# Kernel optimization log

Measured on AMD Instinct MI355X. Metric: run time of the kernel, lower is better.

## Reference

```python
import jax, jax.numpy as jnp
import numpy as np

B, T1, T2, C, H, NIN = 4, 4096, 2048, 512, 8, 3
D = C // H  # head_dim = 64


def setup_inputs() -> dict:
    key = jax.random.key(0)
    ks = jax.random.split(key, 10)
    s = 0.02  # weight init scale
    return {
        "x": jax.random.normal(ks[0], (B, T1, C), jnp.float32),
        "y0": jax.random.normal(ks[1], (B, T2, C), jnp.float32),
        "y1": jax.random.normal(ks[2], (B, T2, C), jnp.float32),
        "y2": jax.random.normal(ks[3], (B, T2, C), jnp.float32),
        "Wq": jax.random.normal(ks[4], (C, C), jnp.float32) * s,
        "bq": jnp.zeros((C,), jnp.float32),
        "Wk": jax.random.normal(ks[5], (NIN, C, C), jnp.float32) * s,
        "bk": jnp.zeros((NIN, C), jnp.float32),
        "Wv": jax.random.normal(ks[6], (NIN, C, C), jnp.float32) * s,
        "bv": jnp.zeros((NIN, C), jnp.float32),
        "Wo": jax.random.normal(ks[7], (C, C), jnp.float32) * s,
        "bo": jnp.zeros((C,), jnp.float32),
    }


def _heads(t, n_head):
    b, n, c = t.shape
    return t.reshape(b, n, n_head, c // n_head).transpose(0, 2, 1, 3)  # [B,H,N,D]


def reference(x, y0, y1, y2, Wq, bq, Wk, bk, Wv, bv, Wo, bo):
    b, t1, c = x.shape
    q = jax.nn.softmax(_heads(x @ Wq.T + bq, H), axis=-1)  # [B,H,T1,D]
    out = q  # note: original initializes accumulator with q itself
    for i, y in enumerate((y0, y1, y2)):
        k = jax.nn.softmax(_heads(y @ Wk[i].T + bk[i], H), axis=-1)  # [B,H,T2,D]
        v = _heads(y @ Wv[i].T + bv[i], H)                            # [B,H,T2,D]
        k_sum = k.sum(axis=-2, keepdims=True)                         # [B,H,1,D]
        D_inv = 1.0 / ((q * k_sum).sum(axis=-1, keepdims=True) + 1e-8)  # [B,H,T1,1]
        context = jnp.einsum('bhnd,bhnv->bhdv', k, v)                 # [B,H,D,D]
        out = out + jnp.einsum('bhqd,bhdv->bhqv', q, context) * D_inv
    out = out.transpose(0, 2, 1, 3).reshape(b, t1, c)
    return out @ Wo.T + bo
```

## Files before the change

kernel.cpp:

```cpp
#include <hip/hip_runtime.h>
#include <stdint.h>

#define B_ 4
#define T1_ 4096
#define T2_ 2048
#define C_ 512
#define H_ 8
#define D_ 64
#define M1_ (B_*T1_)
#define M2_ (B_*T2_)

using f32x4 = __attribute__((ext_vector_type(4))) float;
using bf16x8 = __attribute__((ext_vector_type(8))) __bf16;
using us8 = __attribute__((ext_vector_type(8))) unsigned short;
using us4 = __attribute__((ext_vector_type(4))) unsigned short;

__device__ __forceinline__ unsigned short f2bf(float f){
  unsigned int u = __builtin_bit_cast(unsigned int, f);
  unsigned int r = (u + 0x7fffu + ((u >> 16) & 1u)) >> 16;
  return (unsigned short)r;
}
__device__ __forceinline__ float bf2f(unsigned short u){
  return __builtin_bit_cast(float, ((unsigned int)u) << 16);
}
__device__ __forceinline__ f32x4 mfma16(us8 a, us8 b, f32x4 c){
  return __builtin_amdgcn_mfma_f32_16x16x32_bf16(
      __builtin_bit_cast(bf16x8, a), __builtin_bit_cast(bf16x8, b), c, 0, 0, 0);
}
__device__ __forceinline__ us8 cvt8(f32x4 a, f32x4 b){
  us8 v;
  #pragma unroll
  for (int j = 0; j < 4; ++j){
    v[j]   = __builtin_bit_cast(unsigned short, (__bf16)a[j]);
    v[4+j] = __builtin_bit_cast(unsigned short, (__bf16)b[j]);
  }
  return v;
}

typedef const __attribute__((address_space(1))) unsigned int gu32;
typedef __attribute__((address_space(3))) unsigned int lu32;
__device__ __forceinline__ void gl_lds16(const void* g, void* l){
  __builtin_amdgcn_global_load_lds((gu32*)g, (lu32*)l, 16, 0, 0);
}

#define WAIT_VM(N) asm volatile("s_waitcnt vmcnt(" #N ")" ::: "memory")
#define WAIT_LGKM() asm volatile("s_waitcnt lgkmcnt(0)" ::: "memory")
#define RAW_BAR()  { __builtin_amdgcn_s_barrier(); __builtin_amdgcn_sched_barrier(0); }

__device__ __forceinline__ int swz(int row, int blk){ return blk ^ ((row >> 1) & 3); }

__global__ __launch_bounds__(256) void cvt_bf16_4(const float* __restrict__ p0, const float* __restrict__ p1,
                                                  const float* __restrict__ p2, const float* __restrict__ p3,
                                                  unsigned short* o0, unsigned short* o1,
                                                  unsigned short* o2, unsigned short* o3,
                                                  int n0, int n1, int n2, int n3){
  const float* in; unsigned short* out; int n4;
  switch (blockIdx.y){
    case 0: in = p0; out = o0; n4 = n0; break;
    case 1: in = p1; out = o1; n4 = n1; break;
    case 2: in = p2; out = o2; n4 = n2; break;
    default: in = p3; out = o3; n4 = n3; break;
  }
  int i = blockIdx.x * 256 + threadIdx.x;
  if (i >= n4) return;
  f32x4 v = ((const f32x4*)in)[i];
  us4 o;
  #pragma unroll
  for (int j = 0; j < 4; ++j) o[j] = f2bf(v[j]);
  ((us4*)out)[i] = o;
}

__device__ __forceinline__ void tile_write(unsigned short* tile, const f32x4 (&vals)[4][4],
                                           int wr, int wc, int lr, int lk){
  #pragma unroll
  for (int mt = 0; mt < 4; ++mt)
    #pragma unroll
    for (int nt = 0; nt < 4; ++nt)
      #pragma unroll
      for (int r = 0; r < 4; ++r){
        int row = wr*64 + mt*16 + lk*4 + r;
        int cb  = (wc*128 + nt*32 + lr*2) ^ ((row & 7) << 4);
        *(unsigned short*)((char*)tile + row*256 + cb) = f2bf(vals[mt][nt][r]);
      }
}
__device__ __forceinline__ void tile_write_T(unsigned short* tile, const f32x4 (&vals)[4][4],
                                             int wr, int wc, int lr, int lk){
  #pragma unroll
  for (int mt = 0; mt < 4; ++mt)
    #pragma unroll
    for (int nt = 0; nt < 4; ++nt)
      #pragma unroll
      for (int r = 0; r < 4; ++r){
        int n  = wr*64 + mt*16 + lk*4 + r;
        int ch = wc*64 + nt*16 + lr;
        int cb = (n*2) ^ ((ch & 7) << 4);
        *(unsigned short*)((char*)tile + ch*256 + cb) = f2bf(vals[mt][nt][r]);
      }
}
__device__ __forceinline__ void tile_flush(const unsigned short* tile, unsigned short* g,
                                           size_t row0, int col0, int ldg, int t){
  #pragma unroll
  for (int p = 0; p < 8; ++p){
    int row = p*16 + (t >> 4);
    int cb  = ((t & 15) * 16) ^ ((row & 7) << 4);
    us8 v = *(const us8*)((const char*)tile + row*256 + cb);
    *(us8*)(g + (row0 + row) * (size_t)ldg + col0 + (t & 15) * 8) = v;
  }
}

__global__ __launch_bounds__(256, 3) void proj(const float* __restrict__ xf,
                                               const float* __restrict__ y0f,
                                               const float* __restrict__ y1f,
                                               const float* __restrict__ y2f,
                                               const unsigned short* __restrict__ wqb,
                                               const unsigned short* __restrict__ wkb,
                                               const unsigned short* __restrict__ wvb,
                                               const float* __restrict__ bq,
                                               const float* __restrict__ bk,
                                               const float* __restrict__ bv,
                                               unsigned short* __restrict__ qb,
                                               unsigned short* __restrict__ kbT,
                                               unsigned short* __restrict__ vbT,
                                               float* __restrict__ ksum){
  __shared__ unsigned short smem[24576];
  const int hw = blockIdx.x;
  const int work = (hw & 7) * 256 + (hw >> 3);
  int seg, ii, m0, n0;
  const float* Af;
  const unsigned short* W;
  const float* bias;
  if (work < 512){
    seg = 0; ii = 0;
    m0 = (work >> 2) << 7; n0 = (work & 3) << 7;
    Af = xf; W = wqb; bias = bq;
  } else {
    int r = work - 512;
    int g = r >> 3, s = r & 7;
    ii = g >> 6; m0 = (g & 63) << 7;
    seg = (s < 4) ? 1 : 2;
    n0 = (s & 3) << 7;
    Af = (ii == 0) ? y0f : (ii == 1 ? y1f : y2f);
    W = (seg == 1 ? wkb : wvb) + (size_t)ii*C_*C_;
    bias = (seg == 1 ? bk : bv) + (size_t)ii*C_;
  }
  const int t = threadIdx.x;
  const int w = t >> 6, l = t & 63;
  const int wr = w >> 1, wc = w & 1;
  const int lr = l & 15, lk = l >> 4;
  const int row0 = t >> 2,          b0 = t & 3;
  const int row1 = (t + 256) >> 2,  b1 = t & 3;
  f32x4 acc[4][4] = {};
  f32x4 ar0[4], ar1[4];

#define LOADA(AR, TT) { \
    const float* ap0 = Af + (size_t)(m0+row0)*C_ + (TT)*32 + b0*8; \
    const float* ap1 = Af + (size_t)(m0+row1)*C_ + (TT)*32 + b1*8; \
    AR[0] = *(const f32x4*)ap0; AR[1] = *(const f32x4*)(ap0 + 4); \
    AR[2] = *(const f32x4*)ap1; AR[3] = *(const f32x4*)(ap1 + 4); }
#define DSWA(AR, BUF) { \
    *(us8*)&smem[(BUF)*4096 + row0*32 + swz(row0,b0)*8] = cvt8(AR[0], AR[1]); \
    *(us8*)&smem[(BUF)*4096 + row1*32 + swz(row1,b1)*8] = cvt8(AR[2], AR[3]); }
#define GLW(BUF, TT) { \
    int c=t, row=c>>2; \
    gl_lds16(W + (size_t)(n0+row)*C_ + (TT)*32 + swz(row,c&3)*8, &smem[12288+(BUF)*4096 + c*8]); \
    c=t+256; row=c>>2; \
    gl_lds16(W + (size_t)(n0+row)*C_ + (TT)*32 + swz(row,c&3)*8, &smem[12288+(BUF)*4096 + c*8]); }
#define PCOMP(S, WB) { \
    const unsigned short* sA = &smem[(S)*4096]; \
    const unsigned short* sW = &smem[12288 + (WB)*4096]; \
    us8 af[4], bfr[4]; \
    _Pragma("unroll") \
    for (int mt = 0; mt < 4; ++mt){ int R = wr*64 + mt*16 + lr; af[mt] = *(const us8*)&sA[R*32 + swz(R, lk)*8]; } \
    _Pragma("unroll") \
    for (int nt = 0; nt < 4; ++nt){ int R = wc*64 + nt*16 + lr; bfr[nt] = *(const us8*)&sW[R*32 + swz(R, lk)*8]; } \
    __builtin_amdgcn_s_setprio(1); \
    _Pragma("unroll") \
    for (int mt = 0; mt < 4; ++mt) \
      _Pragma("unroll") \
      for (int nt = 0; nt < 4; ++nt) \
        acc[mt][nt] = mfma16(af[mt], bfr[nt], acc[mt][nt]); \
    __builtin_amdgcn_s_setprio(0); }
#define PSTEP(T, ARW, ARL) { \
    WAIT_VM(2); \
    DSWA(ARW, ((T)+1)%3); \
    LOADA(ARL, (T)+2); \
    GLW(((T)+2)%3, (T)+2); \
    PCOMP((T)%3, (T)%3); \
    WAIT_LGKM(); \
    WAIT_VM(6); \
    RAW_BAR(); }

  LOADA(ar0, 0); GLW(0, 0);
  LOADA(ar1, 1); GLW(1, 1);
  WAIT_VM(8);
  DSWA(ar0, 0);
  WAIT_LGKM();
  WAIT_VM(6);
  RAW_BAR();
  PSTEP(0,  ar1, ar0) PSTEP(1,  ar0, ar1) PSTEP(2,  ar1, ar0) PSTEP(3,  ar0, ar1)
  PSTEP(4,  ar1, ar0) PSTEP(5,  ar0, ar1) PSTEP(6,  ar1, ar0) PSTEP(7,  ar0, ar1)
  PSTEP(8,  ar1, ar0) PSTEP(9,  ar0, ar1) PSTEP(10, ar1, ar0) PSTEP(11, ar0, ar1)
  PSTEP(12, ar1, ar0) PSTEP(13, ar0, ar1)
  {
    WAIT_VM(2);
    DSWA(ar1, 0);
    PCOMP(2, 2);
    WAIT_LGKM();
    WAIT_VM(0);
    RAW_BAR();
  }
  PCOMP(0, 0);
#undef LOADA
#undef DSWA
#undef GLW
#undef PCOMP
#undef PSTEP

  {
    float bc[4];
    #pragma unroll
    for (int nt = 0; nt < 4; ++nt) bc[nt] = bias[n0 + wc*64 + nt*16 + lr];
    #pragma unroll
    for (int mt = 0; mt < 4; ++mt)
      #pragma unroll
      for (int nt = 0; nt < 4; ++nt)
        #pragma unroll
        for (int r = 0; r < 4; ++r) acc[mt][nt][r] += bc[nt];
  }
  if (seg <= 1){
    #pragma unroll
    for (int mt = 0; mt < 4; ++mt)
      #pragma unroll
      for (int r = 0; r < 4; ++r){
        float m = fmaxf(fmaxf(acc[mt][0][r], acc[mt][1][r]), fmaxf(acc[mt][2][r], acc[mt][3][r]));
        #pragma unroll
        for (int s = 1; s < 16; s <<= 1) m = fmaxf(m, __shfl_xor(m, s, 64));
        float sum = 0.f;
        #pragma unroll
        for (int nt = 0; nt < 4; ++nt){
          float e = __expf(acc[mt][nt][r] - m);
          acc[mt][nt][r] = e; sum += e;
        }
        #pragma unroll
        for (int s = 1; s < 16; s <<= 1) sum += __shfl_xor(sum, s, 64);
        float inv = 1.0f / sum;
        #pragma unroll
        for (int nt = 0; nt < 4; ++nt) acc[mt][nt][r] *= inv;
      }
  }
  if (seg == 1){
    const int b = m0 >> 11;
    #pragma unroll
    for (int nt = 0; nt < 4; ++nt){
      float cs = 0.f;
      #pragma unroll
      for (int mt = 0; mt < 4; ++mt)
        #pragma unroll
        for (int r = 0; r < 4; ++r) cs += acc[mt][nt][r];
      cs += __shfl_xor(cs, 16, 64);
      cs += __shfl_xor(cs, 32, 64);
      if (lk == 0)
        atomicAdd(&ksum[((size_t)ii*B_ + b)*C_ + n0 + wc*64 + nt*16 + lr], cs);
    }
  }
  __syncthreads();
  if (seg == 0){
    tile_write(smem, acc, wr, wc, lr, lk);
    __syncthreads();
    tile_flush(smem, qb, m0, n0, C_, t);
  } else {
    tile_write_T(smem, acc, wr, wc, lr, lk);
    __syncthreads();
    const int b = m0 >> 11;
    const int n_base = m0 & 2047;
    unsigned short* gT = (seg == 1 ? kbT : vbT);
    tile_flush(smem, gT, ((size_t)ii*B_ + b)*C_ + n0, n_base, T2_, t);
  }
}

__global__ __launch_bounds__(256) void ctx_mfma(const unsigned short* __restrict__ kbT,
                                                const unsigned short* __restrict__ vbT,
                                                float* __restrict__ part){
  const int bh = blockIdx.x, kc = blockIdx.y, i = blockIdx.z;
  const int b = bh >> 3, h = bh & 7;
  const size_t rowbase = ((size_t)i*B_ + b)*C_ + h*64;
  const unsigned short* kT = kbT + rowbase*T2_;
  const unsigned short* vT = vbT + rowbase*T2_;
  const int t = threadIdx.x;
  const int w = t >> 6, l = t & 63;
  const int qr = w >> 1, qc = w & 1;
  const int lr = l & 15, lk = l >> 4;
  const int n00 = kc * 256;
  f32x4 acc[2][2] = {};
  #pragma unroll
  for (int it = 0; it < 8; ++it){
    const int k0 = n00 + it*32 + lk*8;
    us8 a0 = *(const us8*)(kT + (size_t)(qr*32 +      lr)*T2_ + k0);
    us8 a1 = *(const us8*)(kT + (size_t)(qr*32 + 16 + lr)*T2_ + k0);
    us8 b0 = *(const us8*)(vT + (size_t)(qc*32 +      lr)*T2_ + k0);
    us8 b1 = *(const us8*)(vT + (size_t)(qc*32 + 16 + lr)*T2_ + k0);
    acc[0][0] = mfma16(a0, b0, acc[0][0]);
    acc[0][1] = mfma16(a0, b1, acc[0][1]);
    acc[1][0] = mfma16(a1, b0, acc[1][0]);
    acc[1][1] = mfma16(a1, b1, acc[1][1]);
  }
  float* dst = part + (((size_t)i*8 + kc)*32 + bh)*4096;
  #pragma unroll
  for (int fa = 0; fa < 2; ++fa)
    #pragma unroll
    for (int fb = 0; fb < 2; ++fb){
      int d0 = qr*32 + fa*16 + lk*4;
      int e  = qc*32 + fb*16 + lr;
      *(f32x4*)(dst + e*64 + d0) = acc[fa][fb];
    }
}

__global__ __launch_bounds__(256) void ctx_reduce(const float* __restrict__ part,
                                                  unsigned short* __restrict__ ctxTb){
  const int bh = blockIdx.x, i = blockIdx.y, t = threadIdx.x;
  for (int idx = t; idx < 4096; idx += 256){
    float s = 0.f;
    #pragma unroll
    for (int kc = 0; kc < 8; ++kc)
      s += part[(((size_t)i*8 + kc)*32 + bh)*4096 + idx];
    ctxTb[((size_t)i*32 + bh)*4096 + idx] = f2bf(s);
  }
}

__global__ __launch_bounds__(256) void combine(const unsigned short* __restrict__ qb,
                                               const unsigned short* __restrict__ ctxTb,
                                               const float* __restrict__ ksum,
                                               unsigned short* __restrict__ omid){
  __shared__ unsigned short tile[128*128];
  const int hw = blockIdx.x;
  const int work = (hw & 7) * 64 + (hw >> 3);
  const int m0 = (work & 127) << 7, n0 = (work >> 7) << 7;
  const int t = threadIdx.x;
  const int w = t >> 6, l = t & 63;
  const int wr = w >> 1, wc = w & 1;
  const int lr = l & 15, lk = l >> 4;
  const int b = m0 >> 12;
  const int bh = b*8 + (n0 >> 6) + wc;
  #pragma unroll
  for (int p = 0; p < 8; ++p){
    int idx = p*256 + t;
    int row = idx >> 4, ch = idx & 15;
    gl_lds16(qb + (size_t)(m0+row)*C_ + n0 + (ch ^ (row & 7))*8, &tile[idx*8]);
  }
  WAIT_VM(0);
  __syncthreads();
  us8 afr[4][2];
  #pragma unroll
  for (int mt = 0; mt < 4; ++mt)
    #pragma unroll
    for (int kk = 0; kk < 2; ++kk){
      int row = wr*64 + mt*16 + lr;
      int ch = wc*8 + kk*4 + lk;
      afr[mt][kk] = *(const us8*)((const char*)tile + row*256 + ((ch ^ (row & 7)) << 4));
    }
  f32x4 acc[4][4];
  #pragma unroll
  for (int mt = 0; mt < 4; ++mt)
    #pragma unroll
    for (int nt = 0; nt < 4; ++nt)
      #pragma unroll
      for (int r = 0; r < 4; ++r){
        int row = wr*64 + mt*16 + lk*4 + r;
        int cbyte = wc*128 + nt*32 + lr*2;
        int ch = cbyte >> 4;
        unsigned short v = *(const unsigned short*)((const char*)tile + row*256 +
                            ((ch ^ (row & 7)) << 4) + (cbyte & 15));
        acc[mt][nt][r] = bf2f(v);
      }
  us8 bden[2];
  #pragma unroll
  for (int kk = 0; kk < 2; ++kk){
    us8 tmp = {};
    if (lr < 3){
      const float* kp = ksum + ((size_t)lr*B_ + b)*C_ + n0 + wc*64 + kk*32 + lk*8;
      f32x4 c0 = *(const f32x4*)kp;
      f32x4 c1 = *(const f32x4*)(kp + 4);
      #pragma unroll
      for (int j = 0; j < 4; ++j){ tmp[j] = f2bf(c0[j]); tmp[4+j] = f2bf(c1[j]); }
    }
    bden[kk] = tmp;
  }
  f32x4 den[4] = {};
  #pragma unroll
  for (int mt = 0; mt < 4; ++mt)
    #pragma unroll
    for (int kk = 0; kk < 2; ++kk)
      den[mt] = mfma16(afr[mt][kk], bden[kk], den[mt]);
  #pragma unroll 1
  for (int i = 0; i < 3; ++i){
    f32x4 dinv[4];
    #pragma unroll
    for (int mt = 0; mt < 4; ++mt)
      #pragma unroll
      for (int r = 0; r < 4; ++r)
        dinv[mt][r] = 1.0f / (__shfl(den[mt][r], (l & 48) | i, 64) + 1e-8f);
    #pragma unroll
    for (int nt = 0; nt < 4; ++nt){
      us8 bfr[2];
      #pragma unroll
      for (int kk = 0; kk < 2; ++kk)
        bfr[kk] = *(const us8*)(ctxTb + ((size_t)(i*32 + bh))*4096 + (nt*16 + lr)*64 + kk*32 + lk*8);
      f32x4 p[4] = {};
      #pragma unroll
      for (int mt = 0; mt < 4; ++mt)
        #pragma unroll
        for (int kk = 0; kk < 2; ++kk)
          p[mt] = mfma16(afr[mt][kk], bfr[kk], p[mt]);
      #pragma unroll
      for (int mt = 0; mt < 4; ++mt)
        #pragma unroll
        for (int r = 0; r < 4; ++r)
          acc[mt][nt][r] += p[mt][r] * dinv[mt][r];
    }
  }
  __syncthreads();
  tile_write(tile, acc, wr, wc, lr, lk);
  __syncthreads();
  tile_flush(tile, omid, m0, n0, C_, t);
}

__global__ __launch_bounds__(256, 3) void gemm_bt(const unsigned short* __restrict__ A,
                                                  const unsigned short* __restrict__ Bw,
                                                  const float* __restrict__ bias,
                                                  float* __restrict__ out){
  __shared__ unsigned short smem[3*2*4096];
  const int hw = blockIdx.x;
  const int work = (hw & 7) * 64 + (hw >> 3);
  const int m0 = ((work >> 2) & 127) << 7, n0 = (work & 3) << 7;
  const int t = threadIdx.x;
  const int w = t >> 6, l = t & 63;
  const int wr = w >> 1, wc = w & 1;
  const int lr = l & 15, lk = l >> 4;
  f32x4 acc[4][4] = {};

#define GSTAGE(BB, TT) { \
    int c = t, row = c >> 2; \
    gl_lds16(A  + (size_t)(m0+row)*C_ + (TT)*32 + swz(row, c & 3)*8, &smem[(BB)*8192 + c*8]); \
    gl_lds16(Bw + (size_t)(n0+row)*C_ + (TT)*32 + swz(row, c & 3)*8, &smem[(BB)*8192 + 4096 + c*8]); \
    c = t + 256; row = c >> 2; \
    gl_lds16(A  + (size_t)(m0+row)*C_ + (TT)*32 + swz(row, c & 3)*8, &smem[(BB)*8192 + c*8]); \
    gl_lds16(Bw + (size_t)(n0+row)*C_ + (TT)*32 + swz(row, c & 3)*8, &smem[(BB)*8192 + 4096 + c*8]); }
#define GCOMP(BB) { \
    const unsigned short* sA = &smem[(BB)*8192]; \
    const unsigned short* sB = &smem[(BB)*8192 + 4096]; \
    us8 af[4], bfr[4]; \
    _Pragma("unroll") \
    for (int mt = 0; mt < 4; ++mt){ int R = wr*64 + mt*16 + lr; af[mt] = *(const us8*)&sA[R*32 + swz(R, lk)*8]; } \
    _Pragma("unroll") \
    for (int nt = 0; nt < 4; ++nt){ int R = wc*64 + nt*16 + lr; bfr[nt] = *(const us8*)&sB[R*32 + swz(R, lk)*8]; } \
    __builtin_amdgcn_s_setprio(1); \
    _Pragma("unroll") \
    for (int mt = 0; mt < 4; ++mt) \
      _Pragma("unroll") \
      for (int nt = 0; nt < 4; ++nt) \
        acc[mt][nt] = mfma16(af[mt], bfr[nt], acc[mt][nt]); \
    __builtin_amdgcn_s_setprio(0); }
#define GSTEP(T, N) { \
    if ((T) + 2 < 16) GSTAGE(((T)+2)%3, (T)+2); \
    WAIT_VM(N); \
    RAW_BAR(); \
    GCOMP((T)%3); }

  GSTAGE(0, 0); GSTAGE(1, 1);
  GSTEP(0, 8)  GSTEP(1, 8)  GSTEP(2, 8)  GSTEP(3, 8)
  GSTEP(4, 8)  GSTEP(5, 8)  GSTEP(6, 8)  GSTEP(7, 8)
  GSTEP(8, 8)  GSTEP(9, 8)  GSTEP(10, 8) GSTEP(11, 8)
  GSTEP(12, 8) GSTEP(13, 8) GSTEP(14, 4) GSTEP(15, 0)
#undef GSTAGE
#undef GCOMP
#undef GSTEP

  #pragma unroll
  for (int mt = 0; mt < 4; ++mt)
    #pragma unroll
    for (int nt = 0; nt < 4; ++nt)
      #pragma unroll
      for (int r = 0; r < 4; ++r){
        int row = m0 + wr*64 + mt*16 + lk*4 + r;
        int col = n0 + wc*64 + nt*16 + lr;
        out[(size_t)row*C_ + col] = acc[mt][nt][r] + bias[col];
      }
}

extern "C" void kernel_launch(void* const* d_in, const int* in_sizes, int n_in,
                              void* d_out, int out_size, void* d_ws, size_t ws_size,
                              hipStream_t stream){
  const float* x  = (const float*)d_in[0];
  const float* y0 = (const float*)d_in[1];
  const float* y1 = (const float*)d_in[2];
  const float* y2 = (const float*)d_in[3];
  const float* Wq = (const float*)d_in[4];
  const float* bq = (const float*)d_in[5];
  const float* Wk = (const float*)d_in[6];
  const float* bk = (const float*)d_in[7];
  const float* Wv = (const float*)d_in[8];
  const float* bv = (const float*)d_in[9];
  const float* Wo = (const float*)d_in[10];
  const float* bo = (const float*)d_in[11];

  char* ws = (char*)d_ws;
  size_t off = 0;
  auto alloc = [&](size_t bytes)->char*{
    char* p = ws + off; off += (bytes + 1023) & ~((size_t)1023); return p;
  };
  unsigned short* wqb   = (unsigned short*)alloc((size_t)C_*C_*2);
  unsigned short* wkb   = (unsigned short*)alloc((size_t)3*C_*C_*2);
  unsigned short* wvb   = (unsigned short*)alloc((size_t)3*C_*C_*2);
  unsigned short* wob   = (unsigned short*)alloc((size_t)C_*C_*2);
  unsigned short* qb    = (unsigned short*)alloc((size_t)M1_*C_*2);
  unsigned short* kbT   = (unsigned short*)alloc((size_t)3*B_*C_*T2_*2);
  unsigned short* vbT   = (unsigned short*)alloc((size_t)3*B_*C_*T2_*2);
  float*          ksum  = (float*)alloc((size_t)3*B_*C_*4);
  float*          part  = (float*)alloc((size_t)3*8*32*4096*4);
  unsigned short* ctxTb = (unsigned short*)alloc((size_t)3*32*4096*2);
  unsigned short* omid  = (unsigned short*)alloc((size_t)M1_*C_*2);

  (void)hipMemsetAsync(ksum, 0, (size_t)3*B_*C_*4, stream);

  cvt_bf16_4<<<dim3(3*C_*C_/4/256, 4), 256, 0, stream>>>(
      Wq, Wk, Wv, Wo, wqb, wkb, wvb, wob,
      C_*C_/4, 3*C_*C_/4, 3*C_*C_/4, C_*C_/4);

  proj<<<2048, 256, 0, stream>>>(x, y0, y1, y2, wqb, wkb, wvb, bq, bk, bv, qb, kbT, vbT, ksum);
  ctx_mfma<<<dim3(32, 8, 3), 256, 0, stream>>>(kbT, vbT, part);
  ctx_reduce<<<dim3(32, 3), 256, 0, stream>>>(part, ctxTb);
  combine<<<512, 256, 0, stream>>>(qb, ctxTb, ksum, omid);
  gemm_bt<<<512, 256, 0, stream>>>(omid, wob, bo, (float*)d_out);
}
```

Before: 123.3 us.

## Stream fp32 A tiles directly to LDS and convert to bf16 at fragment load

Result: slower. 140.5 us (+14.0%).

```diff
diff --git a/kernel.cpp b/kernel.cpp
--- a/kernel.cpp
+++ b/kernel.cpp
@@ -44,7 +44,6 @@
 }
 
 #define WAIT_VM(N) asm volatile("s_waitcnt vmcnt(" #N ")" ::: "memory")
-#define WAIT_LGKM() asm volatile("s_waitcnt lgkmcnt(0)" ::: "memory")
 #define RAW_BAR()  { __builtin_amdgcn_s_barrier(); __builtin_amdgcn_sched_barrier(0); }
 
 __device__ __forceinline__ int swz(int row, int blk){ return blk ^ ((row >> 1) & 3); }
@@ -108,21 +107,21 @@
   }
 }
 
-__global__ __launch_bounds__(256, 3) void proj(const float* __restrict__ xf,
-                                               const float* __restrict__ y0f,
-                                               const float* __restrict__ y1f,
-                                               const float* __restrict__ y2f,
-                                               const unsigned short* __restrict__ wqb,
-                                               const unsigned short* __restrict__ wkb,
-                                               const unsigned short* __restrict__ wvb,
-                                               const float* __restrict__ bq,
-                                               const float* __restrict__ bk,
-                                               const float* __restrict__ bv,
-                                               unsigned short* __restrict__ qb,
-                                               unsigned short* __restrict__ kbT,
-                                               unsigned short* __restrict__ vbT,
-                                               float* __restrict__ ksum){
-  __shared__ unsigned short smem[24576];
+__global__ __launch_bounds__(256) void proj(const float* __restrict__ xf,
+                                            const float* __restrict__ y0f,
+                                            const float* __restrict__ y1f,
+                                            const float* __restrict__ y2f,
+                                            const unsigned short* __restrict__ wqb,
+                                            const unsigned short* __restrict__ wkb,
+                                            const unsigned short* __restrict__ wvb,
+                                            const float* __restrict__ bq,
+                                            const float* __restrict__ bk,
+                                            const float* __restrict__ bv,
+                                            unsigned short* __restrict__ qb,
+                                            unsigned short* __restrict__ kbT,
+                                            unsigned short* __restrict__ vbT,
+                                            float* __restrict__ ksum){
+  __shared__ unsigned short smem[36864];
   const int hw = blockIdx.x;
   const int work = (hw & 7) * 256 + (hw >> 3);
   int seg, ii, m0, n0;
@@ -147,30 +146,30 @@
   const int w = t >> 6, l = t & 63;
   const int wr = w >> 1, wc = w & 1;
   const int lr = l & 15, lk = l >> 4;
-  const int row0 = t >> 2,          b0 = t & 3;
-  const int row1 = (t + 256) >> 2,  b1 = t & 3;
   f32x4 acc[4][4] = {};
-  f32x4 ar0[4], ar1[4];
-
-#define LOADA(AR, TT) { \
-    const float* ap0 = Af + (size_t)(m0+row0)*C_ + (TT)*32 + b0*8; \
-    const float* ap1 = Af + (size_t)(m0+row1)*C_ + (TT)*32 + b1*8; \
-    AR[0] = *(const f32x4*)ap0; AR[1] = *(const f32x4*)(ap0 + 4); \
-    AR[2] = *(const f32x4*)ap1; AR[3] = *(const f32x4*)(ap1 + 4); }
-#define DSWA(AR, BUF) { \
-    *(us8*)&smem[(BUF)*4096 + row0*32 + swz(row0,b0)*8] = cvt8(AR[0], AR[1]); \
-    *(us8*)&smem[(BUF)*4096 + row1*32 + swz(row1,b1)*8] = cvt8(AR[2], AR[3]); }
-#define GLW(BUF, TT) { \
-    int c=t, row=c>>2; \
-    gl_lds16(W + (size_t)(n0+row)*C_ + (TT)*32 + swz(row,c&3)*8, &smem[12288+(BUF)*4096 + c*8]); \
-    c=t+256; row=c>>2; \
-    gl_lds16(W + (size_t)(n0+row)*C_ + (TT)*32 + swz(row,c&3)*8, &smem[12288+(BUF)*4096 + c*8]); }
-#define PCOMP(S, WB) { \
-    const unsigned short* sA = &smem[(S)*4096]; \
-    const unsigned short* sW = &smem[12288 + (WB)*4096]; \
+
+#define STAGE(BB, TT) { \
+    _Pragma("unroll") \
+    for (int j = 0; j < 4; ++j){ \
+      int c = t + j*256, row = c >> 3, ch = c & 7; \
+      gl_lds16(Af + (size_t)(m0+row)*C_ + (TT)*32 + ((ch ^ (row & 7)) << 2), \
+               &smem[(BB)*8192 + c*8]); \
+    } \
+    { int c = t, row = c >> 2; \
+      gl_lds16(W + (size_t)(n0+row)*C_ + (TT)*32 + swz(row, c & 3)*8, &smem[24576 + (BB)*4096 + c*8]); \
+      c = t + 256; row = c >> 2; \
+      gl_lds16(W + (size_t)(n0+row)*C_ + (TT)*32 + swz(row, c & 3)*8, &smem[24576 + (BB)*4096 + c*8]); } }
+#define PCOMP(BB) { \
+    const float* sAf = (const float*)&smem[(BB)*8192]; \
+    const unsigned short* sW = &smem[24576 + (BB)*4096]; \
     us8 af[4], bfr[4]; \
     _Pragma("unroll") \
-    for (int mt = 0; mt < 4; ++mt){ int R = wr*64 + mt*16 + lr; af[mt] = *(const us8*)&sA[R*32 + swz(R, lk)*8]; } \
+    for (int mt = 0; mt < 4; ++mt){ \
+      int R = wr*64 + mt*16 + lr, x = R & 7; \
+      f32x4 a0 = *(const f32x4*)(sAf + R*32 + (((2*lk)     ^ x) << 2)); \
+      f32x4 a1 = *(const f32x4*)(sAf + R*32 + (((2*lk + 1) ^ x) << 2)); \
+      af[mt] = cvt8(a0, a1); \
+    } \
     _Pragma("unroll") \
     for (int nt = 0; nt < 4; ++nt){ int R = wc*64 + nt*16 + lr; bfr[nt] = *(const us8*)&sW[R*32 + swz(R, lk)*8]; } \
     __builtin_amdgcn_s_setprio(1); \
@@ -180,41 +179,23 @@
       for (int nt = 0; nt < 4; ++nt) \
         acc[mt][nt] = mfma16(af[mt], bfr[nt], acc[mt][nt]); \
     __builtin_amdgcn_s_setprio(0); }
-#define PSTEP(T, ARW, ARL) { \
-    WAIT_VM(2); \
-    DSWA(ARW, ((T)+1)%3); \
-    LOADA(ARL, (T)+2); \
-    GLW(((T)+2)%3, (T)+2); \
-    PCOMP((T)%3, (T)%3); \
-    WAIT_LGKM(); \
-    WAIT_VM(6); \
-    RAW_BAR(); }
-
-  LOADA(ar0, 0); GLW(0, 0);
-  LOADA(ar1, 1); GLW(1, 1);
-  WAIT_VM(8);
-  DSWA(ar0, 0);
-  WAIT_LGKM();
-  WAIT_VM(6);
+
+  STAGE(0, 0);
+  int cur = 0;
+  #pragma unroll 1
+  for (int tt = 0; tt < 15; ++tt){
+    int nxt = (cur == 2) ? 0 : cur + 1;
+    STAGE(nxt, tt + 1);
+    WAIT_VM(6);
+    RAW_BAR();
+    PCOMP(cur);
+    cur = nxt;
+  }
+  WAIT_VM(0);
   RAW_BAR();
-  PSTEP(0,  ar1, ar0) PSTEP(1,  ar0, ar1) PSTEP(2,  ar1, ar0) PSTEP(3,  ar0, ar1)
-  PSTEP(4,  ar1, ar0) PSTEP(5,  ar0, ar1) PSTEP(6,  ar1, ar0) PSTEP(7,  ar0, ar1)
-  PSTEP(8,  ar1, ar0) PSTEP(9,  ar0, ar1) PSTEP(10, ar1, ar0) PSTEP(11, ar0, ar1)
-  PSTEP(12, ar1, ar0) PSTEP(13, ar0, ar1)
-  {
-    WAIT_VM(2);
-    DSWA(ar1, 0);
-    PCOMP(2, 2);
-    WAIT_LGKM();
-    WAIT_VM(0);
-    RAW_BAR();
-  }
-  PCOMP(0, 0);
-#undef LOADA
-#undef DSWA
-#undef GLW
+  PCOMP(cur);
+#undef STAGE
 #undef PCOMP
-#undef PSTEP
 
   {
     float bc[4];
```
